# Kernel optimization log

Measured on AMD Instinct MI355X. Metric: run time of the kernel, lower is better.

## Reference

```python
import jax, jax.numpy as jnp
import numpy as np

N_NODES = 50000
N_EDGES = 800000
N_GRAPHS = 128


def _gcn_conv(x, W, b, src, dst, n_nodes):
    # PyG GCNConv: h = x @ W; add self-loops; symmetric norm; aggregate; + bias
    h = x @ W  # [N, out]
    loop = jnp.arange(n_nodes, dtype=src.dtype)
    src_all = jnp.concatenate([src, loop])  # source (row)
    dst_all = jnp.concatenate([dst, loop])  # target (col)
    ones = jnp.ones(src_all.shape[0], dtype=h.dtype)
    deg = jax.ops.segment_sum(ones, dst_all, num_segments=n_nodes)  # in-degree w/ self loops
    dis = jnp.where(deg > 0, jax.lax.rsqrt(deg), 0.0)
    norm = dis[src_all] * dis[dst_all]  # [E+N]
    msg = norm[:, None] * h[src_all]  # [E+N, out]
    out = jax.ops.segment_sum(msg, dst_all, num_segments=n_nodes)
    return out + b


def setup_inputs() -> dict:
    key = jax.random.key(0)
    ks = jax.random.split(key, 7)
    x = jax.random.normal(ks[0], (N_NODES, 4), dtype=jnp.float32)
    edge_index = jax.random.randint(ks[1], (2, N_EDGES), 0, N_NODES, dtype=jnp.int64)
    batch = jnp.sort(jax.random.randint(ks[2], (N_NODES,), 0, N_GRAPHS, dtype=jnp.int64))
    # Glorot-ish init for the linear weights, zeros for bias (PyG default)
    W1 = jax.random.normal(ks[3], (4, 64), dtype=jnp.float32) * (1.0 / np.sqrt(4))
    b1 = jnp.zeros((64,), dtype=jnp.float32)
    W2 = jax.random.normal(ks[4], (64, 64), dtype=jnp.float32) * (1.0 / np.sqrt(64))
    b2 = jnp.zeros((64,), dtype=jnp.float32)
    return {"x": x, "edge_index": edge_index, "batch": batch, "num_graphs": N_GRAPHS,
            "W1": W1, "b1": b1, "W2": W2, "b2": b2}


def reference(x, edge_index, batch, num_graphs, W1, b1, W2, b2):
    src, dst = edge_index[0], edge_index[1]
    n = x.shape[0]
    h = jax.nn.relu(_gcn_conv(x, W1, b1, src, dst, n))
    h = jax.nn.relu(_gcn_conv(h, W2, b2, src, dst, n))
    # global_mean_pool: segment mean over graph ids
    sums = jax.ops.segment_sum(h, batch, num_segments=num_graphs)  # [G, 64]
    cnts = jax.ops.segment_sum(jnp.ones((n,), dtype=h.dtype), batch, num_segments=num_graphs)
    return sums / jnp.maximum(cnts, 1.0)[:, None]
```

## Files before the change

### kernel.cpp

```cpp
#include <hip/hip_runtime.h>
#include <hip/hip_fp16.h>

#define NG 128
#define CHUNK 4096

__device__ __forceinline__ int wave_iscan(int v, int lane) {
#pragma unroll
  for (int off = 1; off < 64; off <<= 1) {
    int u = __shfl_up(v, off, 64);
    if (lane >= off) v += u;
  }
  return v;
}


__global__ void bsum_kernel(const int* __restrict__ src, int* __restrict__ bsum, int M) {
  __shared__ int wsum[4];
  int tid = threadIdx.x, lane = tid & 63, wid = tid >> 6;
  int i = blockIdx.x * 256 + tid;
  int v = (i < M) ? src[i] : 0;
  int inc = wave_iscan(v, lane);
  if (lane == 63) wsum[wid] = inc;
  __syncthreads();
  if (tid == 0) bsum[blockIdx.x] = wsum[0] + wsum[1] + wsum[2] + wsum[3];
}

__global__ void bscan_kernel(int* __restrict__ bsum, int nb) {
  __shared__ int wsum[16];
  int tid = threadIdx.x, lane = tid & 63, wid = tid >> 6;
  int v = (tid < nb) ? bsum[tid] : 0;
  int inc = wave_iscan(v, lane);
  if (lane == 63) wsum[wid] = inc;
  __syncthreads();
  if (tid == 0) {
    int a = 0;
#pragma unroll
    for (int w = 0; w < 16; ++w) { int t = wsum[w]; wsum[w] = a; a += t; }
  }
  __syncthreads();
  if (tid < nb) bsum[tid] = inc - v + wsum[wid];
}

__global__ void offadd_kernel(int* __restrict__ off, const int* __restrict__ bsum, int M) {
  __shared__ int wsum[4];
  int tid = threadIdx.x, lane = tid & 63, wid = tid >> 6;
  int i = blockIdx.x * 256 + tid;
  int v = (i < M) ? off[i] : 0;
  int inc = wave_iscan(v, lane);
  if (lane == 63) wsum[wid] = inc;
  __syncthreads();
  if (tid == 0) {
    int a = bsum[blockIdx.x];
#pragma unroll
    for (int w = 0; w < 4; ++w) { int t = wsum[w]; wsum[w] = a; a += t; }
  }
  __syncthreads();
  if (i < M) off[i] = inc - v + wsum[wid];
}


__global__ void hist_kernel(const int* __restrict__ ei, int E, int nblkE, int K,
                            int* __restrict__ off) {
  __shared__ int lh[256];
  int tid = threadIdx.x, blk = blockIdx.x;
  lh[tid] = 0;
  __syncthreads();
  int e0 = blk * CHUNK;
  for (int i = tid; i < CHUNK; i += 256) {
    int e = e0 + i;
    if (e < E) atomicAdd(&lh[ei[E + e] >> 8], 1);
  }
  __syncthreads();
  if (tid < K) off[tid * nblkE + blk] = lh[tid];
}

__global__ void part_kernel(const int* __restrict__ ei, int E, int nblkE, int K,
                            const int* __restrict__ off, unsigned int* __restrict__ epack) {
  __shared__ int lcur[256];
  int tid = threadIdx.x, blk = blockIdx.x;
  if (tid < K) lcur[tid] = off[tid * nblkE + blk];
  __syncthreads();
  int e0 = blk * CHUNK;
  for (int i = tid; i < CHUNK; i += 256) {
    int e = e0 + i;
    if (e < E) {
      unsigned int s = (unsigned int)ei[e], d = (unsigned int)ei[E + e];
      int pos = atomicAdd(&lcur[d >> 8], 1);
      epack[pos] = (s << 8) | (d & 255u);
    }
  }
}

__global__ void csr2_kernel(const int* __restrict__ off, int nblkE, int K,
                            const unsigned int* __restrict__ epack,
                            const float* __restrict__ x, int* __restrict__ deg,
                            int* __restrict__ rowptr, float* __restrict__ dis,
                            float* __restrict__ xs, unsigned short* __restrict__ esrc,
                            int N, int E) {
  __shared__ int lcnt[256];
  __shared__ int lcur[256];
  __shared__ int wsum[4];
  int tid = threadIdx.x, b = blockIdx.x;
  int lane = tid & 63, wid = tid >> 6;
  lcnt[tid] = 0;
  __syncthreads();
  int be0 = off[b * nblkE];
  int be1 = (b + 1 < K) ? off[(b + 1) * nblkE] : E;
  for (int i = be0 + tid; i < be1; i += 256) atomicAdd(&lcnt[epack[i] & 255u], 1);
  __syncthreads();
  int v = lcnt[tid];
  int inc = wave_iscan(v, lane);
  if (lane == 63) wsum[wid] = inc;
  __syncthreads();
  if (tid == 0) {
    int a = be0;
#pragma unroll
    for (int w = 0; w < 4; ++w) { int t = wsum[w]; wsum[w] = a; a += t; }
  }
  __syncthreads();
  int exc = inc - v + wsum[wid];
  lcur[tid] = exc;
  int node = (b << 8) + tid;
  if (node < N) {
    rowptr[node] = exc;
    deg[node] = v;
    float di = rsqrtf((float)v + 1.0f);
    dis[node] = di;
    float4 xv = ((const float4*)x)[node];
    ((float4*)xs)[node] = make_float4(di * xv.x, di * xv.y, di * xv.z, di * xv.w);
  }
  __syncthreads();
  for (int i = be0 + tid; i < be1; i += 256) {
    unsigned int pk = epack[i];
    int pos = atomicAdd(&lcur[pk & 255u], 1);
    esrc[pos] = (unsigned short)(pk >> 8);
  }
}

__global__ void l1_kernel(const int* __restrict__ rowptr, const int* __restrict__ deg,
                          const unsigned short* __restrict__ esrc, const float* __restrict__ xs,
                          const float* __restrict__ x, const float* __restrict__ dis,
                          const float* __restrict__ W1, const float* __restrict__ b1,
                          __half* __restrict__ h1p, int N) {
  int tid = threadIdx.x;
  int lane = tid & 63, wid = tid >> 6;
  int d = __builtin_amdgcn_readfirstlane(blockIdx.x * 4 + wid);
  if (d >= N) return;
  float di = dis[d];
  int p = __builtin_amdgcn_readfirstlane(rowptr[d]);
  int n = __builtin_amdgcn_readfirstlane(deg[d]);
  float a0 = 0.f, a1 = 0.f, a2 = 0.f, a3 = 0.f;
  for (int k = lane; k < n; k += 64) {
    int e = esrc[p + k];
    float4 v = ((const float4*)xs)[e];
    a0 += v.x; a1 += v.y; a2 += v.z; a3 += v.w;
  }
  if (lane == 0) {
    float4 xv = ((const float4*)x)[d];
    a0 = fmaf(di, xv.x, a0); a1 = fmaf(di, xv.y, a1);
    a2 = fmaf(di, xv.z, a2); a3 = fmaf(di, xv.w, a3);
  }
#pragma unroll
  for (int off = 1; off < 64; off <<= 1) {
    a0 += __shfl_xor(a0, off, 64);
    a1 += __shfl_xor(a1, off, 64);
    a2 += __shfl_xor(a2, off, 64);
    a3 += __shfl_xor(a3, off, 64);
  }
  a0 *= di; a1 *= di; a2 *= di; a3 *= di;
  float o = b1[lane] + a0 * W1[lane] + a1 * W1[64 + lane] + a2 * W1[128 + lane] + a3 * W1[192 + lane];
  h1p[(size_t)d * 64 + lane] = __float2half(di * fmaxf(o, 0.0f));
}

__global__ void __launch_bounds__(256)
l2_kernel(const int* __restrict__ rowptr, const int* __restrict__ deg,
          const unsigned short* __restrict__ esrc, const __half* __restrict__ h1p,
          const float* __restrict__ dis, const float* __restrict__ W2,
          const float* __restrict__ b2, const int* __restrict__ batch,
          float* __restrict__ gsum, int N) {
  __shared__ __align__(16) unsigned short ebuf[4][64];
  __shared__ float vbuf[4][64];
  __shared__ float obuf[4][64];
  __shared__ int gbuf[4];
  int tid = threadIdx.x;
  int lane = tid & 63, wid = tid >> 6;
  int d0 = blockIdx.x * 4 + wid;
  bool valid = d0 < N;
  int d = __builtin_amdgcn_readfirstlane(valid ? d0 : N - 1);
  float di = dis[d];
  float acc0 = __half2float(h1p[(size_t)d * 64 + lane]);
  float acc1 = 0.f, acc2 = 0.f, acc3 = 0.f;
  float acc4 = 0.f, acc5 = 0.f, acc6 = 0.f, acc7 = 0.f;
  int p = __builtin_amdgcn_readfirstlane(rowptr[d]);
  int n = __builtin_amdgcn_readfirstlane(deg[d]);
  for (int base = 0; base < n; base += 64) {
    int m64 = n - base;
    if (m64 > 64) m64 = 64;
    ebuf[wid][lane] = esrc[p + base + ((lane < m64) ? lane : (m64 - 1))];
    for (int k = 0; k < m64; k += 16) {
      uint4 wA = *(const uint4*)&ebuf[wid][k];
      uint4 wB = *(const uint4*)&ebuf[wid][k + 8];
      unsigned int ua0 = wA.x, ua1 = wA.y, ua2 = wA.z, ua3 = wA.w;
      unsigned int ub0 = wB.x, ub1 = wB.y, ub2 = wB.z, ub3 = wB.w;
#pragma unroll
      for (int i = 0; i < 8; ++i) {
        unsigned int u = (i == 0) ? ua0 : (i == 1) ? ua1 : (i == 2) ? ua2 : (i == 3) ? ua3
                       : (i == 4) ? ub0 : (i == 5) ? ub1 : (i == 6) ? ub2 : ub3;
        int ea = (int)(u & 0xffffu), eb = (int)(u >> 16);
        float ma = (k + 2 * i < m64) ? 1.0f : 0.0f;
        float mb = (k + 2 * i + 1 < m64) ? 1.0f : 0.0f;
        float va = __half2float(h1p[(size_t)ea * 64 + lane]);
        float vb = __half2float(h1p[(size_t)eb * 64 + lane]);
        switch (i & 3) {
          case 0: acc0 = fmaf(ma, va, acc0); acc1 = fmaf(mb, vb, acc1); break;
          case 1: acc2 = fmaf(ma, va, acc2); acc3 = fmaf(mb, vb, acc3); break;
          case 2: acc4 = fmaf(ma, va, acc4); acc5 = fmaf(mb, vb, acc5); break;
          case 3: acc6 = fmaf(ma, va, acc6); acc7 = fmaf(mb, vb, acc7); break;
        }
      }
    }
  }
  float v = di * (((acc0 + acc1) + (acc2 + acc3)) + ((acc4 + acc5) + (acc6 + acc7)));
  vbuf[wid][lane] = v;
  float o = b2[lane];
  const float4* vb4 = (const float4*)vbuf[wid];
#pragma unroll
  for (int kk = 0; kk < 16; ++kk) {
    float4 vv = vb4[kk];
    o = fmaf(vv.x, W2[(kk * 4 + 0) * 64 + lane], o);
    o = fmaf(vv.y, W2[(kk * 4 + 1) * 64 + lane], o);
    o = fmaf(vv.z, W2[(kk * 4 + 2) * 64 + lane], o);
    o = fmaf(vv.w, W2[(kk * 4 + 3) * 64 + lane], o);
  }
  obuf[wid][lane] = fmaxf(o, 0.0f);
  if (lane == 0) gbuf[wid] = valid ? batch[d] : -1;
  __syncthreads();
  if (wid == 0) {
    float s = 0.0f;
    int cur = gbuf[0];
#pragma unroll
    for (int r = 0; r < 4; ++r) {
      int g = gbuf[r];
      if (g != cur) {
        if (cur >= 0) atomicAdd(&gsum[cur * 64 + lane], s);
        s = 0.0f;
        cur = g;
      }
      if (g >= 0) s += obuf[r][lane];
    }
    if (cur >= 0) atomicAdd(&gsum[cur * 64 + lane], s);
  }
}


__device__ __forceinline__ int lbound(const int* __restrict__ a, int n, int v) {
  int lo = 0, hi = n;
  while (lo < hi) {
    int mid = (lo + hi) >> 1;
    if (a[mid] < v) lo = mid + 1; else hi = mid;
  }
  return lo;
}

__global__ void out_kernel(const float* __restrict__ gsum, const int* __restrict__ batch,
                           int N, float* __restrict__ out) {
  int t = blockIdx.x * blockDim.x + threadIdx.x;
  if (t >= NG * 64) return;
  int g = t >> 6;
  int cnt = lbound(batch, N, g + 1) - lbound(batch, N, g);
  out[t] = gsum[t] / fmaxf((float)cnt, 1.0f);
}


extern "C" void kernel_launch(void* const* d_in, const int* in_sizes, int n_in,
                              void* d_out, int out_size, void* d_ws, size_t ws_size,
                              hipStream_t stream) {
  const float* x = (const float*)d_in[0];
  const int* ei = (const int*)d_in[1];
  const int* batch = (const int*)d_in[2];
  const float* W1 = (const float*)d_in[4];
  const float* b1 = (const float*)d_in[5];
  const float* W2 = (const float*)d_in[6];
  const float* b2 = (const float*)d_in[7];

  const int N = in_sizes[0] / 4;
  const int E = in_sizes[1] / 2;
  const int K = (N + 255) >> 8;
  const int nblkE = (E + CHUNK - 1) / CHUNK;
  const int M2 = K * nblkE;
  const int NB2 = (M2 + 255) / 256;

  float* gsum = (float*)d_ws;
  int* deg = (int*)(gsum + 64 * NG);
  int* rowptr = deg + N;
  float* xs = (float*)(rowptr + N);
  float* dis = xs + (size_t)4 * N;
  __half* h1p = (__half*)(dis + N);
  unsigned short* esrc = (unsigned short*)(dis + N + (size_t)32 * N);
  int* off = (int*)(esrc + E);
  int* bsum2 = off + M2;
  unsigned int* epack = (unsigned int*)(bsum2 + 1024);

  hipMemsetAsync(d_ws, 0, (size_t)64 * NG * 4, stream);

  const int B = 256;
  hist_kernel<<<nblkE, 256, 0, stream>>>(ei, E, nblkE, K, off);
  bsum_kernel<<<NB2, 256, 0, stream>>>(off, bsum2, M2);
  bscan_kernel<<<1, 1024, 0, stream>>>(bsum2, NB2);
  offadd_kernel<<<NB2, 256, 0, stream>>>(off, bsum2, M2);
  part_kernel<<<nblkE, 256, 0, stream>>>(ei, E, nblkE, K, off, epack);
  csr2_kernel<<<K, 256, 0, stream>>>(off, nblkE, K, epack, x, deg, rowptr, dis, xs, esrc, N, E);
  l1_kernel<<<(N + 3) / 4, 256, 0, stream>>>(rowptr, deg, esrc, xs, x, dis, W1, b1, h1p, N);
  l2_kernel<<<(N + 3) / 4, 256, 0, stream>>>(rowptr, deg, esrc, h1p, dis, W2, b2, batch, gsum, N);
  out_kernel<<<(NG * 64 + B - 1) / B, B, 0, stream>>>(gsum, batch, N, (float*)d_out);
}
```

Before: 110.8 us.

## Quantize layer-1 activations to uint8 with global max scale for layer-2 gather

Layer 1 now computes a per-block max of its output. A new single-block reduction turns that into a global scale, and a new kernel quantizes the fp16 activations to unsigned 8-bit. Layer 2 gathers the 8-bit values and applies the scale once at the end, halving the bytes fetched per neighbour in the dominant random gather. This adds two kernel launches and a full extra pass over the activations, and it cuts precision to 8 bits with a single global scale, which may go beyond tolerance. Launch bounds were also set to 8 waves per SIMD on both layer kernels.

Measured after the change: 119.4 us. 1.08x slower.

```diff
diff --git a/kernel.cpp b/kernel.cpp
--- a/kernel.cpp
+++ b/kernel.cpp
@@ -137,15 +137,17 @@
   }
 }
 
-__global__ void l1_kernel(const int* __restrict__ rowptr, const int* __restrict__ deg,
-                          const unsigned short* __restrict__ esrc, const float* __restrict__ xs,
-                          const float* __restrict__ x, const float* __restrict__ dis,
-                          const float* __restrict__ W1, const float* __restrict__ b1,
-                          __half* __restrict__ h1p, int N) {
+__global__ void __launch_bounds__(256, 8)
+l1_kernel(const int* __restrict__ rowptr, const int* __restrict__ deg,
+          const unsigned short* __restrict__ esrc, const float* __restrict__ xs,
+          const float* __restrict__ x, const float* __restrict__ dis,
+          const float* __restrict__ W1, const float* __restrict__ b1,
+          __half* __restrict__ h1p, float* __restrict__ blockmax, int N) {
+  __shared__ float bm[4];
   int tid = threadIdx.x;
   int lane = tid & 63, wid = tid >> 6;
-  int d = __builtin_amdgcn_readfirstlane(blockIdx.x * 4 + wid);
-  if (d >= N) return;
+  int d0 = blockIdx.x * 4 + wid;
+  int d = __builtin_amdgcn_readfirstlane((d0 < N) ? d0 : (N - 1));
   float di = dis[d];
   int p = __builtin_amdgcn_readfirstlane(rowptr[d]);
   int n = __builtin_amdgcn_readfirstlane(deg[d]);
@@ -169,15 +171,60 @@
   }
   a0 *= di; a1 *= di; a2 *= di; a3 *= di;
   float o = b1[lane] + a0 * W1[lane] + a1 * W1[64 + lane] + a2 * W1[128 + lane] + a3 * W1[192 + lane];
-  h1p[(size_t)d * 64 + lane] = __float2half(di * fmaxf(o, 0.0f));
-}
-
-__global__ void __launch_bounds__(256)
+  float h = di * fmaxf(o, 0.0f);
+  h1p[(size_t)d * 64 + lane] = __float2half(h);
+  float wm = h;
+#pragma unroll
+  for (int off = 1; off < 64; off <<= 1) wm = fmaxf(wm, __shfl_xor(wm, off, 64));
+  if (lane == 0) bm[wid] = wm;
+  __syncthreads();
+  if (tid == 0) blockmax[blockIdx.x] = fmaxf(fmaxf(bm[0], bm[1]), fmaxf(bm[2], bm[3]));
+}
+
+__global__ void qs_kernel(const float* __restrict__ blockmax, int nb, float* __restrict__ qs) {
+  __shared__ float wm[16];
+  int tid = threadIdx.x, lane = tid & 63, wid = tid >> 6;
+  float m = 0.0f;
+  for (int i = tid; i < nb; i += 1024) m = fmaxf(m, blockmax[i]);
+#pragma unroll
+  for (int off = 1; off < 64; off <<= 1) m = fmaxf(m, __shfl_xor(m, off, 64));
+  if (lane == 0) wm[wid] = m;
+  __syncthreads();
+  if (tid == 0) {
+    float M = 0.0f;
+#pragma unroll
+    for (int w = 0; w < 16; ++w) M = fmaxf(M, wm[w]);
+    qs[0] = M * (1.0f / 255.0f);
+    qs[1] = (M > 0.0f) ? (255.0f / M) : 0.0f;
+  }
+}
+
+__global__ void quant_kernel(const __half* __restrict__ h1p, const float* __restrict__ qs,
+                             unsigned char* __restrict__ h1q, int M8) {
+  int i = blockIdx.x * 256 + threadIdx.x;
+  if (i >= M8) return;
+  float isc = qs[1];
+  uint4 w = ((const uint4*)h1p)[i];
+  unsigned int r0 = 0, r1 = 0;
+#pragma unroll
+  for (int j = 0; j < 4; ++j) {
+    unsigned int u = (j == 0) ? w.x : (j == 1) ? w.y : (j == 2) ? w.z : w.w;
+    __half2 h2 = *(__half2*)&u;
+    float2 f = __half22float2(h2);
+    unsigned int qa = (unsigned int)(int)rintf(f.x * isc);
+    unsigned int qb = (unsigned int)(int)rintf(f.y * isc);
+    if (j < 2) r0 |= (qa << (16 * j)) | (qb << (16 * j + 8));
+    else       r1 |= (qa << (16 * (j - 2))) | (qb << (16 * (j - 2) + 8));
+  }
+  ((uint2*)h1q)[i] = make_uint2(r0, r1);
+}
+
+__global__ void __launch_bounds__(256, 8)
 l2_kernel(const int* __restrict__ rowptr, const int* __restrict__ deg,
-          const unsigned short* __restrict__ esrc, const __half* __restrict__ h1p,
-          const float* __restrict__ dis, const float* __restrict__ W2,
-          const float* __restrict__ b2, const int* __restrict__ batch,
-          float* __restrict__ gsum, int N) {
+          const unsigned short* __restrict__ esrc, const unsigned char* __restrict__ h1q,
+          const float* __restrict__ qs, const float* __restrict__ dis,
+          const float* __restrict__ W2, const float* __restrict__ b2,
+          const int* __restrict__ batch, float* __restrict__ gsum, int N) {
   __shared__ __align__(16) unsigned short ebuf[4][64];
   __shared__ float vbuf[4][64];
   __shared__ float obuf[4][64];
@@ -188,7 +235,8 @@
   bool valid = d0 < N;
   int d = __builtin_amdgcn_readfirstlane(valid ? d0 : N - 1);
   float di = dis[d];
-  float acc0 = __half2float(h1p[(size_t)d * 64 + lane]);
+  float qscale = qs[0];
+  float acc0 = (float)h1q[(size_t)d * 64 + lane];
   float acc1 = 0.f, acc2 = 0.f, acc3 = 0.f;
   float acc4 = 0.f, acc5 = 0.f, acc6 = 0.f, acc7 = 0.f;
   int p = __builtin_amdgcn_readfirstlane(rowptr[d]);
@@ -209,8 +257,8 @@
         int ea = (int)(u & 0xffffu), eb = (int)(u >> 16);
         float ma = (k + 2 * i < m64) ? 1.0f : 0.0f;
         float mb = (k + 2 * i + 1 < m64) ? 1.0f : 0.0f;
-        float va = __half2float(h1p[(size_t)ea * 64 + lane]);
-        float vb = __half2float(h1p[(size_t)eb * 64 + lane]);
+        float va = (float)h1q[(size_t)ea * 64 + lane];
+        float vb = (float)h1q[(size_t)eb * 64 + lane];
         switch (i & 3) {
           case 0: acc0 = fmaf(ma, va, acc0); acc1 = fmaf(mb, vb, acc1); break;
           case 1: acc2 = fmaf(ma, va, acc2); acc3 = fmaf(mb, vb, acc3); break;
@@ -220,7 +268,8 @@
       }
     }
   }
-  float v = di * (((acc0 + acc1) + (acc2 + acc3)) + ((acc4 + acc5) + (acc6 + acc7)));
+  float v = di * qscale *
+            (((acc0 + acc1) + (acc2 + acc3)) + ((acc4 + acc5) + (acc6 + acc7)));
   vbuf[wid][lane] = v;
   float o = b2[lane];
   const float4* vb4 = (const float4*)vbuf[wid];
@@ -289,6 +338,7 @@
   const int nblkE = (E + CHUNK - 1) / CHUNK;
   const int M2 = K * nblkE;
   const int NB2 = (M2 + 255) / 256;
+  const int NBL1 = (N + 3) / 4;
 
   float* gsum = (float*)d_ws;
   int* deg = (int*)(gsum + 64 * NG);
@@ -296,10 +346,13 @@
   float* xs = (float*)(rowptr + N);
   float* dis = xs + (size_t)4 * N;
   __half* h1p = (__half*)(dis + N);
-  unsigned short* esrc = (unsigned short*)(dis + N + (size_t)32 * N);
+  unsigned char* h1q = (unsigned char*)(dis + N + (size_t)32 * N);
+  unsigned short* esrc = (unsigned short*)(h1q + (size_t)64 * N);
   int* off = (int*)(esrc + E);
   int* bsum2 = off + M2;
-  unsigned int* epack = (unsigned int*)(bsum2 + 1024);
+  float* blockmax = (float*)(bsum2 + 1024);
+  float* qs = blockmax + NBL1;
+  unsigned int* epack = (unsigned int*)(qs + 2);
 
   hipMemsetAsync(d_ws, 0, (size_t)64 * NG * 4, stream);
 
@@ -310,7 +363,9 @@
   offadd_kernel<<<NB2, 256, 0, stream>>>(off, bsum2, M2);
   part_kernel<<<nblkE, 256, 0, stream>>>(ei, E, nblkE, K, off, epack);
   csr2_kernel<<<K, 256, 0, stream>>>(off, nblkE, K, epack, x, deg, rowptr, dis, xs, esrc, N, E);
-  l1_kernel<<<(N + 3) / 4, 256, 0, stream>>>(rowptr, deg, esrc, xs, x, dis, W1, b1, h1p, N);
-  l2_kernel<<<(N + 3) / 4, 256, 0, stream>>>(rowptr, deg, esrc, h1p, dis, W2, b2, batch, gsum, N);
+  l1_kernel<<<NBL1, 256, 0, stream>>>(rowptr, deg, esrc, xs, x, dis, W1, b1, h1p, blockmax, N);
+  qs_kernel<<<1, 1024, 0, stream>>>(blockmax, NBL1, qs);
+  quant_kernel<<<(8 * N + B - 1) / B, B, 0, stream>>>(h1p, qs, h1q, 8 * N);
+  l2_kernel<<<(N + 3) / 4, 256, 0, stream>>>(rowptr, deg, esrc, h1q, qs, dis, W2, b2, batch, gsum, N);
   out_kernel<<<(NG * 64 + B - 1) / B, B, 0, stream>>>(gsum, batch, N, (float*)d_out);
 }
```

## Gather 8 neighbor rows per wave iteration with 16-byte half loads in layer-2 aggregation

Applied to the files above, without the earlier changes.

Layer-2 aggregation now splits each wave into 8 groups of 8 lanes. Each group loads one neighbor's 64-half feature row, with each lane taking 8 halves via one uint4 load, so a single wave iteration covers 8 edges. Partial sums are then combined with cross-group shuffles before the dense W2 projection. This replaces per-lane 2-byte scattered loads with wider vectorized loads, at the cost of extra shuffle reductions and more registers. Launch bounds with an occupancy hint of 8 are also added to both aggregation kernels.

Measured after the change: 109.3 us. No clear change (-1.4%).

```diff
diff --git a/kernel.cpp b/kernel.cpp
--- a/kernel.cpp
+++ b/kernel.cpp
@@ -137,11 +137,12 @@
   }
 }
 
-__global__ void l1_kernel(const int* __restrict__ rowptr, const int* __restrict__ deg,
-                          const unsigned short* __restrict__ esrc, const float* __restrict__ xs,
-                          const float* __restrict__ x, const float* __restrict__ dis,
-                          const float* __restrict__ W1, const float* __restrict__ b1,
-                          __half* __restrict__ h1p, int N) {
+__global__ void __launch_bounds__(256, 8)
+l1_kernel(const int* __restrict__ rowptr, const int* __restrict__ deg,
+          const unsigned short* __restrict__ esrc, const float* __restrict__ xs,
+          const float* __restrict__ x, const float* __restrict__ dis,
+          const float* __restrict__ W1, const float* __restrict__ b1,
+          __half* __restrict__ h1p, int N) {
   int tid = threadIdx.x;
   int lane = tid & 63, wid = tid >> 6;
   int d = __builtin_amdgcn_readfirstlane(blockIdx.x * 4 + wid);
@@ -172,7 +173,7 @@
   h1p[(size_t)d * 64 + lane] = __float2half(di * fmaxf(o, 0.0f));
 }
 
-__global__ void __launch_bounds__(256)
+__global__ void __launch_bounds__(256, 8)
 l2_kernel(const int* __restrict__ rowptr, const int* __restrict__ deg,
           const unsigned short* __restrict__ esrc, const __half* __restrict__ h1p,
           const float* __restrict__ dis, const float* __restrict__ W2,
@@ -184,44 +185,53 @@
   __shared__ int gbuf[4];
   int tid = threadIdx.x;
   int lane = tid & 63, wid = tid >> 6;
+  int g = lane >> 3, c = lane & 7;
   int d0 = blockIdx.x * 4 + wid;
   bool valid = d0 < N;
   int d = __builtin_amdgcn_readfirstlane(valid ? d0 : N - 1);
   float di = dis[d];
-  float acc0 = __half2float(h1p[(size_t)d * 64 + lane]);
-  float acc1 = 0.f, acc2 = 0.f, acc3 = 0.f;
-  float acc4 = 0.f, acc5 = 0.f, acc6 = 0.f, acc7 = 0.f;
   int p = __builtin_amdgcn_readfirstlane(rowptr[d]);
   int n = __builtin_amdgcn_readfirstlane(deg[d]);
+  float a0, a1, a2, a3, a4, a5, a6, a7;
+  {
+    float ms = (g == 0) ? 1.0f : 0.0f;
+    uint4 w = *(const uint4*)(h1p + (size_t)d * 64 + 8 * c);
+    float2 f0 = __half22float2(*(__half2*)&w.x);
+    float2 f1 = __half22float2(*(__half2*)&w.y);
+    float2 f2 = __half22float2(*(__half2*)&w.z);
+    float2 f3 = __half22float2(*(__half2*)&w.w);
+    a0 = ms * f0.x; a1 = ms * f0.y; a2 = ms * f1.x; a3 = ms * f1.y;
+    a4 = ms * f2.x; a5 = ms * f2.y; a6 = ms * f3.x; a7 = ms * f3.y;
+  }
   for (int base = 0; base < n; base += 64) {
     int m64 = n - base;
     if (m64 > 64) m64 = 64;
     ebuf[wid][lane] = esrc[p + base + ((lane < m64) ? lane : (m64 - 1))];
-    for (int k = 0; k < m64; k += 16) {
-      uint4 wA = *(const uint4*)&ebuf[wid][k];
-      uint4 wB = *(const uint4*)&ebuf[wid][k + 8];
-      unsigned int ua0 = wA.x, ua1 = wA.y, ua2 = wA.z, ua3 = wA.w;
-      unsigned int ub0 = wB.x, ub1 = wB.y, ub2 = wB.z, ub3 = wB.w;
-#pragma unroll
-      for (int i = 0; i < 8; ++i) {
-        unsigned int u = (i == 0) ? ua0 : (i == 1) ? ua1 : (i == 2) ? ua2 : (i == 3) ? ua3
-                       : (i == 4) ? ub0 : (i == 5) ? ub1 : (i == 6) ? ub2 : ub3;
-        int ea = (int)(u & 0xffffu), eb = (int)(u >> 16);
-        float ma = (k + 2 * i < m64) ? 1.0f : 0.0f;
-        float mb = (k + 2 * i + 1 < m64) ? 1.0f : 0.0f;
-        float va = __half2float(h1p[(size_t)ea * 64 + lane]);
-        float vb = __half2float(h1p[(size_t)eb * 64 + lane]);
-        switch (i & 3) {
-          case 0: acc0 = fmaf(ma, va, acc0); acc1 = fmaf(mb, vb, acc1); break;
-          case 1: acc2 = fmaf(ma, va, acc2); acc3 = fmaf(mb, vb, acc3); break;
-          case 2: acc4 = fmaf(ma, va, acc4); acc5 = fmaf(mb, vb, acc5); break;
-          case 3: acc6 = fmaf(ma, va, acc6); acc7 = fmaf(mb, vb, acc7); break;
-        }
-      }
+    for (int k = 0; k < m64; k += 8) {
+      int e = ebuf[wid][k + g];
+      float m = (k + g < m64) ? 1.0f : 0.0f;
+      uint4 w = *(const uint4*)(h1p + (size_t)e * 64 + 8 * c);
+      float2 f0 = __half22float2(*(__half2*)&w.x);
+      float2 f1 = __half22float2(*(__half2*)&w.y);
+      float2 f2 = __half22float2(*(__half2*)&w.z);
+      float2 f3 = __half22float2(*(__half2*)&w.w);
+      a0 = fmaf(m, f0.x, a0); a1 = fmaf(m, f0.y, a1);
+      a2 = fmaf(m, f1.x, a2); a3 = fmaf(m, f1.y, a3);
+      a4 = fmaf(m, f2.x, a4); a5 = fmaf(m, f2.y, a5);
+      a6 = fmaf(m, f3.x, a6); a7 = fmaf(m, f3.y, a7);
     }
   }
-  float v = di * (((acc0 + acc1) + (acc2 + acc3)) + ((acc4 + acc5) + (acc6 + acc7)));
-  vbuf[wid][lane] = v;
+#pragma unroll
+  for (int off = 8; off < 64; off <<= 1) {
+    a0 += __shfl_xor(a0, off, 64); a1 += __shfl_xor(a1, off, 64);
+    a2 += __shfl_xor(a2, off, 64); a3 += __shfl_xor(a3, off, 64);
+    a4 += __shfl_xor(a4, off, 64); a5 += __shfl_xor(a5, off, 64);
+    a6 += __shfl_xor(a6, off, 64); a7 += __shfl_xor(a7, off, 64);
+  }
+  if (g == 0) {
+    *(float4*)&vbuf[wid][8 * c] = make_float4(di * a0, di * a1, di * a2, di * a3);
+    *(float4*)&vbuf[wid][8 * c + 4] = make_float4(di * a4, di * a5, di * a6, di * a7);
+  }
   float o = b2[lane];
   const float4* vb4 = (const float4*)vbuf[wid];
 #pragma unroll
@@ -240,13 +250,13 @@
     int cur = gbuf[0];
 #pragma unroll
     for (int r = 0; r < 4; ++r) {
-      int g = gbuf[r];
-      if (g != cur) {
+      int gg = gbuf[r];
+      if (gg != cur) {
         if (cur >= 0) atomicAdd(&gsum[cur * 64 + lane], s);
         s = 0.0f;
-        cur = g;
+        cur = gg;
       }
-      if (g >= 0) s += obuf[r][lane];
+      if (gg >= 0) s += obuf[r][lane];
     }
     if (cur >= 0) atomicAdd(&gsum[cur * 64 + lane], s);
   }
```

## Restructure layer-1 aggregation to one block per 256-node chunk with LDS atomics

Applied to the files above, without the earlier changes.

The layer-1 kernel now gives each block 256 consecutive destination nodes. The block walks their contiguous edge range edge-parallel, finds each edge's destination with a binary search over the local row pointers, and accumulates the 4-wide features with shared-memory atomics. Each thread then computes its node's 64 outputs from W1 and b1 cached in LDS and writes them as packed 16-byte half stores. This replaces one wave per node, which left most lanes idle at about 16 edges per node and needed a full shuffle reduction. The cost is LDS atomic contention and the search overhead. Separately, l2_kernel gains a launch_bounds occupancy hint of 8.

New measurement: 134.9 us. 21.7% more time.

```diff
diff --git a/kernel.cpp b/kernel.cpp
--- a/kernel.cpp
+++ b/kernel.cpp
@@ -137,42 +137,71 @@
   }
 }
 
-__global__ void l1_kernel(const int* __restrict__ rowptr, const int* __restrict__ deg,
-                          const unsigned short* __restrict__ esrc, const float* __restrict__ xs,
-                          const float* __restrict__ x, const float* __restrict__ dis,
-                          const float* __restrict__ W1, const float* __restrict__ b1,
-                          __half* __restrict__ h1p, int N) {
-  int tid = threadIdx.x;
-  int lane = tid & 63, wid = tid >> 6;
-  int d = __builtin_amdgcn_readfirstlane(blockIdx.x * 4 + wid);
-  if (d >= N) return;
-  float di = dis[d];
-  int p = __builtin_amdgcn_readfirstlane(rowptr[d]);
-  int n = __builtin_amdgcn_readfirstlane(deg[d]);
-  float a0 = 0.f, a1 = 0.f, a2 = 0.f, a3 = 0.f;
-  for (int k = lane; k < n; k += 64) {
-    int e = esrc[p + k];
-    float4 v = ((const float4*)xs)[e];
-    a0 += v.x; a1 += v.y; a2 += v.z; a3 += v.w;
-  }
-  if (lane == 0) {
-    float4 xv = ((const float4*)x)[d];
-    a0 = fmaf(di, xv.x, a0); a1 = fmaf(di, xv.y, a1);
-    a2 = fmaf(di, xv.z, a2); a3 = fmaf(di, xv.w, a3);
-  }
-#pragma unroll
-  for (int off = 1; off < 64; off <<= 1) {
-    a0 += __shfl_xor(a0, off, 64);
-    a1 += __shfl_xor(a1, off, 64);
-    a2 += __shfl_xor(a2, off, 64);
-    a3 += __shfl_xor(a3, off, 64);
-  }
-  a0 *= di; a1 *= di; a2 *= di; a3 *= di;
-  float o = b1[lane] + a0 * W1[lane] + a1 * W1[64 + lane] + a2 * W1[128 + lane] + a3 * W1[192 + lane];
-  h1p[(size_t)d * 64 + lane] = __float2half(di * fmaxf(o, 0.0f));
-}
-
 __global__ void __launch_bounds__(256)
+l1_kernel(const int* __restrict__ rowptr, const unsigned short* __restrict__ esrc,
+          const float* __restrict__ xs, const float* __restrict__ x,
+          const float* __restrict__ dis, const float* __restrict__ W1,
+          const float* __restrict__ b1, __half* __restrict__ h1p,
+          int N, int E, int K) {
+  __shared__ int lrp[256];
+  __shared__ float agg[256][4];
+  __shared__ float w1s[256];
+  __shared__ float b1s[64];
+  int tid = threadIdx.x, b = blockIdx.x;
+  int node = (b << 8) + tid;
+  lrp[tid] = (node < N) ? rowptr[node] : E;
+  agg[tid][0] = 0.f; agg[tid][1] = 0.f; agg[tid][2] = 0.f; agg[tid][3] = 0.f;
+  w1s[tid] = W1[tid];
+  if (tid < 64) b1s[tid] = b1[tid];
+  __syncthreads();
+  int be0 = lrp[0];
+  int be1 = ((b + 1) < K) ? rowptr[(b + 1) << 8] : E;
+  for (int i = be0 + tid; i < be1; i += 256) {
+    int s = esrc[i];
+    float4 v = ((const float4*)xs)[s];
+    int lo = 0;
+#pragma unroll
+    for (int st = 128; st >= 1; st >>= 1) {
+      int c = lo + st;
+      if (c < 256 && lrp[c] <= i) lo = c;
+    }
+    atomicAdd(&agg[lo][0], v.x);
+    atomicAdd(&agg[lo][1], v.y);
+    atomicAdd(&agg[lo][2], v.z);
+    atomicAdd(&agg[lo][3], v.w);
+  }
+  __syncthreads();
+  if (node < N) {
+    float di = dis[node];
+    float4 xv = ((const float4*)x)[node];
+    float a0 = di * (agg[tid][0] + di * xv.x);
+    float a1 = di * (agg[tid][1] + di * xv.y);
+    float a2 = di * (agg[tid][2] + di * xv.z);
+    float a3 = di * (agg[tid][3] + di * xv.w);
+    __half* row = h1p + (size_t)node * 64;
+#pragma unroll
+    for (int jj = 0; jj < 8; ++jj) {
+      float o[8];
+#pragma unroll
+      for (int t = 0; t < 8; ++t) {
+        int j = jj * 8 + t;
+        float oo = b1s[j] + a0 * w1s[j] + a1 * w1s[64 + j] + a2 * w1s[128 + j] +
+                   a3 * w1s[192 + j];
+        o[t] = di * fmaxf(oo, 0.0f);
+      }
+      __half2 p0 = __floats2half2_rn(o[0], o[1]);
+      __half2 p1 = __floats2half2_rn(o[2], o[3]);
+      __half2 p2 = __floats2half2_rn(o[4], o[5]);
+      __half2 p3 = __floats2half2_rn(o[6], o[7]);
+      uint4 pk;
+      pk.x = *(unsigned int*)&p0; pk.y = *(unsigned int*)&p1;
+      pk.z = *(unsigned int*)&p2; pk.w = *(unsigned int*)&p3;
+      *(uint4*)(row + jj * 8) = pk;
+    }
+  }
+}
+
+__global__ void __launch_bounds__(256, 8)
 l2_kernel(const int* __restrict__ rowptr, const int* __restrict__ deg,
           const unsigned short* __restrict__ esrc, const __half* __restrict__ h1p,
           const float* __restrict__ dis, const float* __restrict__ W2,
@@ -310,7 +339,7 @@
   offadd_kernel<<<NB2, 256, 0, stream>>>(off, bsum2, M2);
   part_kernel<<<nblkE, 256, 0, stream>>>(ei, E, nblkE, K, off, epack);
   csr2_kernel<<<K, 256, 0, stream>>>(off, nblkE, K, epack, x, deg, rowptr, dis, xs, esrc, N, E);
-  l1_kernel<<<(N + 3) / 4, 256, 0, stream>>>(rowptr, deg, esrc, xs, x, dis, W1, b1, h1p, N);
+  l1_kernel<<<K, 256, 0, stream>>>(rowptr, esrc, xs, x, dis, W1, b1, h1p, N, E, K);
   l2_kernel<<<(N + 3) / 4, 256, 0, stream>>>(rowptr, deg, esrc, h1p, dis, W2, b2, batch, gsum, N);
   out_kernel<<<(NG * 64 + B - 1) / B, B, 0, stream>>>(gsum, batch, N, (float*)d_out);
 }
```
